# Optimization experiments

Measured on AMD Instinct MI355X. Metric: run time of the kernel, lower is better.

Reference implementation:

```python
import jax, jax.numpy as jnp
from jax import lax
import numpy as np

D_MODEL, D_STATE, D_CONV, EXPAND = 1024, 16, 4, 2
D_INNER = EXPAND * D_MODEL          # 2048
DT_RANK = D_MODEL // 16             # 64
B_SZ, L_SEQ = 2, 2048


def setup_inputs() -> dict:
    key = jax.random.key(0)
    ks = jax.random.split(key, 8)
    x = jax.random.normal(ks[0], (B_SZ, L_SEQ, D_MODEL), jnp.float32)
    inp = {
        "x": x,
        "ln_g": jnp.ones((D_MODEL,), jnp.float32),
        "ln_b": jnp.zeros((D_MODEL,), jnp.float32),
        # fan-in scaled weights for numerical sanity
        "W_in": jax.random.normal(ks[1], (2 * D_INNER, D_MODEL), jnp.float32) / np.sqrt(D_MODEL),
        "conv_w": jax.random.normal(ks[2], (D_INNER, D_CONV), jnp.float32) / np.sqrt(D_CONV),
        "conv_b": jnp.zeros((D_INNER,), jnp.float32),
        "W_xp": jax.random.normal(ks[3], (DT_RANK + 2 * D_STATE, D_INNER), jnp.float32) / np.sqrt(D_INNER),
        "W_dt": jax.random.normal(ks[4], (D_INNER, DT_RANK), jnp.float32) / np.sqrt(DT_RANK),
        "b_dt": jax.random.normal(ks[5], (D_INNER,), jnp.float32) * 0.1 - 4.0,  # softplus(dt) small, like mamba init
        # S4D-real init: A = -exp(A_log), A_log = log(1..d_state)
        "A_log": jnp.broadcast_to(jnp.log(jnp.arange(1, D_STATE + 1, dtype=jnp.float32)), (D_INNER, D_STATE)).copy(),
        "D": jnp.ones((D_INNER,), jnp.float32),
        "W_out": jax.random.normal(ks[6], (D_MODEL, D_INNER), jnp.float32) / np.sqrt(D_INNER),
    }
    return inp


def _selective_scan(u, dt, A, Bm, Cm, Dvec):
    # u, dt: (B, L, d_inner); Bm, Cm: (B, L, d_state); A: (d_inner, d_state)
    def step(h, inputs):
        u_t, dt_t, B_t, C_t = inputs                      # (B,di),(B,di),(B,n),(B,n)
        dA = jnp.exp(dt_t[:, :, None] * A[None])          # (B,di,n), in (0,1) since A<0
        dBu = (dt_t * u_t)[:, :, None] * B_t[:, None, :]  # (B,di,n)
        h = dA * h + dBu
        y = jnp.einsum('bdn,bn->bd', h, C_t)
        return h, y
    xs = (u.transpose(1, 0, 2), dt.transpose(1, 0, 2),
          Bm.transpose(1, 0, 2), Cm.transpose(1, 0, 2))
    h0 = jnp.zeros((u.shape[0], u.shape[2], A.shape[1]), u.dtype)
    _, ys = lax.scan(step, h0, xs)
    return ys.transpose(1, 0, 2) + u * Dvec               # (B, L, d_inner)


def reference(x, ln_g, ln_b, W_in, conv_w, conv_b, W_xp, W_dt, b_dt, A_log, D, W_out):
    d_inner, d_conv = conv_w.shape
    dt_rank = W_dt.shape[1]
    d_state = A_log.shape[1]
    # pre-LayerNorm
    mu = jnp.mean(x, axis=-1, keepdims=True)
    var = jnp.mean(jnp.square(x - mu), axis=-1, keepdims=True)
    xn = (x - mu) * lax.rsqrt(var + 1e-5) * ln_g + ln_b
    # input projection -> (B, L, 2*d_inner)
    xz = jnp.einsum('bld,ed->ble', xn, W_in)
    u, z = jnp.split(xz, 2, axis=-1)
    # causal depthwise conv over time
    u_c = lax.conv_general_dilated(
        u.transpose(0, 2, 1),                 # (B, d_inner, L)
        conv_w[:, None, :],                   # (d_inner, 1, d_conv)
        window_strides=(1,), padding=[(d_conv - 1, 0)],
        feature_group_count=d_inner)
    u_c = jax.nn.silu((u_c + conv_b[None, :, None]).transpose(0, 2, 1))  # (B, L, d_inner)
    # data-dependent dt, B, C
    x_dbl = jnp.einsum('bld,ed->ble', u_c, W_xp)
    dt, Bm, Cm = jnp.split(x_dbl, [dt_rank, dt_rank + d_state], axis=-1)
    dt = jax.nn.softplus(jnp.einsum('blr,dr->bld', dt, W_dt) + b_dt)
    A = -jnp.exp(A_log)
    y = _selective_scan(u_c, dt, A, Bm, Cm, D)
    y = y * jax.nn.silu(z)
    out = jnp.einsum('ble,de->bld', y, W_out)
    return x + out
```

## Files before the change

### kernel.cpp

```cpp
#include <hip/hip_runtime.h>

typedef __bf16 bf16x8 __attribute__((ext_vector_type(8)));
typedef float  f32x4  __attribute__((ext_vector_type(4)));

#define LOG2E 1.44269504088896f

__device__ __forceinline__ float bfl(unsigned short s) {
    return __uint_as_float(((unsigned int)s) << 16);
}
__device__ __forceinline__ unsigned short f2bf(float f) {
    unsigned int x = __float_as_uint(f);
    x += 0x7fffu + ((x >> 16) & 1u);
    return (unsigned short)(x >> 16);
}
__device__ __forceinline__ float fexp2(float x) { return __builtin_amdgcn_exp2f(x); }
__device__ __forceinline__ float fexp(float x)  { return __builtin_amdgcn_exp2f(x * LOG2E); }
__device__ __forceinline__ float frcp(float x)  { return __builtin_amdgcn_rcpf(x); }
__device__ __forceinline__ float silu_f(float x) {
    return x * frcp(1.f + fexp2(-x * LOG2E));
}
__device__ __forceinline__ void gl_lds(const unsigned short* g, unsigned short* l) {
    __builtin_amdgcn_global_load_lds(
        (__attribute__((address_space(1))) const void*)g,
        (__attribute__((address_space(3))) void*)l, 16, 0, 0);
}

#define BSZ   2
#define LSEQ  2048
#define DMODEL 1024
#define DI    2048
#define DS    16
#define NCH   64
#define CL    32

#define WI_N   4194304
#define WXP_N  196608
#define WDT_N  131072
#define WOUT_N 2097152
#define WSEG1  (WI_N)
#define WSEG2  (WI_N + WXP_N)
#define WSEG3  (WI_N + WXP_N + WDT_N)
#define WTOT   (WI_N + WXP_N + WDT_N + WOUT_N)

__global__ __launch_bounds__(256) void cvt_weights(
    const float* __restrict__ w0, const float* __restrict__ w1,
    const float* __restrict__ w2, const float* __restrict__ w3,
    unsigned short* __restrict__ dst)
{
    const size_t e0 = ((size_t)blockIdx.x * 256 + threadIdx.x) * 8;
    if (e0 >= WTOT) return;
    const float* src;
    size_t off;
    if      (e0 < WSEG1) { src = w0; off = e0; }
    else if (e0 < WSEG2) { src = w1; off = e0 - WSEG1; }
    else if (e0 < WSEG3) { src = w2; off = e0 - WSEG2; }
    else                 { src = w3; off = e0 - WSEG3; }
    float4 a = *(const float4*)(src + off);
    float4 b = *(const float4*)(src + off + 4);
    ushort4 lo, hi;
    lo.x = f2bf(a.x); lo.y = f2bf(a.y); lo.z = f2bf(a.z); lo.w = f2bf(a.w);
    hi.x = f2bf(b.x); hi.y = f2bf(b.y); hi.z = f2bf(b.z); hi.w = f2bf(b.w);
    *(ushort4*)(dst + e0) = lo;
    *(ushort4*)(dst + e0 + 4) = hi;
}

__global__ __launch_bounds__(256) void ln_kernel(
    const float* __restrict__ x,
    const float* __restrict__ g,
    const float* __restrict__ b,
    unsigned short* __restrict__ xn)
{
    const int row = blockIdx.x;
    const int tid = threadIdx.x;
    const int lane = tid & 63, wv = tid >> 6;
    const float* xp = x + (size_t)row * DMODEL;

    float4 v = ((const float4*)xp)[tid];
    float s = v.x + v.y + v.z + v.w;
    float q = v.x*v.x + v.y*v.y + v.z*v.z + v.w*v.w;
    #pragma unroll
    for (int o = 32; o > 0; o >>= 1) {
        s += __shfl_down(s, o);
        q += __shfl_down(q, o);
    }
    __shared__ float ss[4], sq[4];
    if (lane == 0) { ss[wv] = s; sq[wv] = q; }
    __syncthreads();
    s = ss[0] + ss[1] + ss[2] + ss[3];
    q = sq[0] + sq[1] + sq[2] + sq[3];
    const float mu  = s * (1.f / DMODEL);
    const float var = q * (1.f / DMODEL) - mu * mu;
    const float rs  = rsqrtf(var + 1e-5f);

    float4 gv = ((const float4*)g)[tid];
    float4 bv = ((const float4*)b)[tid];
    ushort4 o;
    o.x = f2bf((v.x - mu) * rs * gv.x + bv.x);
    o.y = f2bf((v.y - mu) * rs * gv.y + bv.y);
    o.z = f2bf((v.z - mu) * rs * gv.z + bv.z);
    o.w = f2bf((v.w - mu) * rs * gv.w + bv.w);
    ((ushort4*)(xn + (size_t)row * DMODEL))[tid] = o;
}

template<int EPI, int LOGM>
__global__ __launch_bounds__(512, 2) void gemm_pipe256(
    const unsigned short* __restrict__ A,
    const unsigned short* __restrict__ Bw,
    void* __restrict__ Cout,
    const void* __restrict__ aux0,
    int K, int ldc)
{
    __shared__ unsigned short As[2][256 * 64];
    __shared__ unsigned short Bs[2][256 * 64];
    const int tid  = threadIdx.x;
    const int lane = tid & 63;
    const int wid  = tid >> 6;
    const int wm   = (wid >> 2) * 128;
    const int wn   = (wid & 3) * 64;

    const int nwg = gridDim.x;
    const int id  = blockIdx.x;
    const int swz = (id & 7) * (nwg >> 3) + (id >> 3);
    const int bx  = swz & ((1 << LOGM) - 1);
    const int by  = swz >> LOGM;
    const size_t am0 = (size_t)bx * 256;
    const size_t bn0 = (size_t)by * 256;

    const int srow  = lane >> 3;
    const int sslot = (lane & 7) ^ srow;
    const unsigned short* gA = A  + (am0 + wid * 8 + srow) * (size_t)K + sslot * 8;
    const unsigned short* gB = Bw + (bn0 + wid * 8 + srow) * (size_t)K + sslot * 8;

    const int NT = K >> 6;

#define STAGE256(buf, ko)                                                      \
    {   _Pragma("unroll")                                                      \
        for (int j = 0; j < 4; ++j)                                            \
            gl_lds(gA + (size_t)(j * 64) * K + (ko), &As[buf][(j * 64 + wid * 8) * 64]); \
        _Pragma("unroll")                                                      \
        for (int j = 0; j < 4; ++j)                                            \
            gl_lds(gB + (size_t)(j * 64) * K + (ko), &Bs[buf][(j * 64 + wid * 8) * 64]); }

    STAGE256(0, 0)
    STAGE256(1, 64)

    f32x4 acc[8][4];
    f32x4 z4 = {0.f, 0.f, 0.f, 0.f};
    #pragma unroll
    for (int i = 0; i < 8; ++i)
        #pragma unroll
        for (int j = 0; j < 4; ++j) acc[i][j] = z4;

    const int lr  = lane & 15;
    const int lq  = lane >> 4;
    const int key = lr & 7;

#define RD_A(dst, q)                                                           \
    _Pragma("unroll")                                                          \
    for (int i = 0; i < 2; ++i)                                                \
        _Pragma("unroll")                                                      \
        for (int ks = 0; ks < 2; ++ks)                                         \
            dst[i][ks] = *(const bf16x8*)&As[cur][(wm + ((q) * 2 + i) * 16 + lr) * 64 \
                                                  + (((ks * 4 + lq) ^ key) * 8)];

#define MFMA_Q(src, q)                                                         \
    _Pragma("unroll")                                                          \
    for (int i = 0; i < 2; ++i)                                                \
        _Pragma("unroll")                                                      \
        for (int fn = 0; fn < 4; ++fn) {                                       \
            acc[(q) * 2 + i][fn] = __builtin_amdgcn_mfma_f32_16x16x32_bf16(    \
                src[i][0], bfv[fn][0], acc[(q) * 2 + i][fn], 0, 0, 0);         \
            acc[(q) * 2 + i][fn] = __builtin_amdgcn_mfma_f32_16x16x32_bf16(    \
                src[i][1], bfv[fn][1], acc[(q) * 2 + i][fn], 0, 0, 0);         }

    for (int t = 0; t < NT; ++t) {
        const int cur = t & 1;
        if (t < NT - 1) asm volatile("s_waitcnt vmcnt(8)" ::: "memory");
        else            asm volatile("s_waitcnt vmcnt(0)" ::: "memory");
        __builtin_amdgcn_s_barrier();
        __builtin_amdgcn_sched_barrier(0);

        bf16x8 bfv[4][2], fA[2][2], fB[2][2];
        #pragma unroll
        for (int fn = 0; fn < 4; ++fn)
            #pragma unroll
            for (int ks = 0; ks < 2; ++ks)
                bfv[fn][ks] = *(const bf16x8*)&Bs[cur][(wn + fn * 16 + lr) * 64
                                                        + (((ks * 4 + lq) ^ key) * 8)];
        RD_A(fA, 0)
        asm volatile("s_waitcnt lgkmcnt(0)" ::: "memory");
        __builtin_amdgcn_sched_barrier(0);

        RD_A(fB, 1)
        __builtin_amdgcn_s_setprio(1);
        MFMA_Q(fA, 0)
        __builtin_amdgcn_s_setprio(0);
        asm volatile("s_waitcnt lgkmcnt(0)" ::: "memory");
        __builtin_amdgcn_sched_barrier(0);

        RD_A(fA, 2)
        __builtin_amdgcn_s_setprio(1);
        MFMA_Q(fB, 1)
        __builtin_amdgcn_s_setprio(0);
        asm volatile("s_waitcnt lgkmcnt(0)" ::: "memory");
        __builtin_amdgcn_sched_barrier(0);

        RD_A(fB, 3)
        __builtin_amdgcn_s_setprio(1);
        MFMA_Q(fA, 2)
        __builtin_amdgcn_s_setprio(0);
        asm volatile("s_waitcnt lgkmcnt(0)" ::: "memory");
        __builtin_amdgcn_sched_barrier(0);

        __builtin_amdgcn_s_barrier();
        if (t + 2 < NT) {
            STAGE256(cur, (size_t)(t + 2) * 64)
        }
        __builtin_amdgcn_s_setprio(1);
        MFMA_Q(fB, 3)
        __builtin_amdgcn_s_setprio(0);
    }
#undef RD_A
#undef MFMA_Q
#undef STAGE256

    const int er = lq * 4;
    const int ec = lr;
    #pragma unroll
    for (int fm = 0; fm < 8; ++fm) {
        #pragma unroll
        for (int fn = 0; fn < 4; ++fn) {
            const size_t col = bn0 + wn + fn * 16 + ec;
            #pragma unroll
            for (int r = 0; r < 4; ++r) {
                const size_t row = am0 + wm + fm * 16 + er + r;
                float v = acc[fm][fn][r];
                if constexpr (EPI == 0) {
                    ((unsigned short*)Cout)[row * ldc + col] = f2bf(v);
                } else {
                    float t2 = v + ((const float*)aux0)[row * ldc + col];
                    ((float*)Cout)[row * ldc + col] = t2;
                }
            }
        }
    }
}

template<int BM, int BN, int EPI, int LOG_NBXM>
__global__ __launch_bounds__(256) void gemm_lds(
    const unsigned short* __restrict__ A,
    const unsigned short* __restrict__ Bw,
    void* __restrict__ Cout,
    const void* __restrict__ aux0,
    int K, int ldc)
{
    constexpr int FM = BM / 32;
    constexpr int FN = BN / 32;
    __shared__ unsigned short As[BM * 64];
    __shared__ unsigned short Bs[BN * 64];
    const int tid  = threadIdx.x;
    const int lane = tid & 63;
    const int wv   = tid >> 6;
    const int wm   = (wv >> 1) * (BM / 2);
    const int wn   = (wv & 1)  * (BN / 2);

    const int nwg = gridDim.x;
    const int id  = blockIdx.x;
    const int swz = (id & 7) * (nwg >> 3) + (id >> 3);
    const int bx  = swz & ((1 << LOG_NBXM) - 1);
    const int by  = swz >> LOG_NBXM;

    f32x4 acc[FM][FN];
    f32x4 z4 = {0.f, 0.f, 0.f, 0.f};
    #pragma unroll
    for (int i = 0; i < FM; ++i)
        #pragma unroll
        for (int j = 0; j < FN; ++j) acc[i][j] = z4;

    const size_t am0 = (size_t)bx * BM;
    const size_t bn0 = (size_t)by * BN;
    const int srow  = lane >> 3;
    const int scol  = (lane & 7) * 8;

    for (int k0 = 0; k0 < K; k0 += 64) {
        __syncthreads();
        #pragma unroll
        for (int i = 0; i < BM / 32; ++i) {
            const int rb = (wv * (BM / 32) + i) * 8;
            gl_lds(&A[(am0 + rb + srow) * (size_t)K + k0 + scol], &As[rb * 64]);
        }
        #pragma unroll
        for (int i = 0; i < BN / 32; ++i) {
            const int rb = (wv * (BN / 32) + i) * 8;
            gl_lds(&Bw[(bn0 + rb + srow) * (size_t)K + k0 + scol], &Bs[rb * 64]);
        }
        __syncthreads();
        const int lr = lane & 15, lk = (lane >> 4) * 8;
        #pragma unroll
        for (int ks = 0; ks < 2; ++ks) {
            bf16x8 af[FM], bfv[FN];
            #pragma unroll
            for (int fm = 0; fm < FM; ++fm)
                af[fm] = *(const bf16x8*)&As[(wm + fm * 16 + lr) * 64 + ks * 32 + lk];
            #pragma unroll
            for (int fn = 0; fn < FN; ++fn)
                bfv[fn] = *(const bf16x8*)&Bs[(wn + fn * 16 + lr) * 64 + ks * 32 + lk];
            #pragma unroll
            for (int fm = 0; fm < FM; ++fm)
                #pragma unroll
                for (int fn = 0; fn < FN; ++fn)
                    acc[fm][fn] = __builtin_amdgcn_mfma_f32_16x16x32_bf16(
                        af[fm], bfv[fn], acc[fm][fn], 0, 0, 0);
        }
    }

    const int er = (lane >> 4) * 4;
    const int ec = lane & 15;
    #pragma unroll
    for (int fm = 0; fm < FM; ++fm) {
        #pragma unroll
        for (int fn = 0; fn < FN; ++fn) {
            const size_t col = bn0 + wn + fn * 16 + ec;
            #pragma unroll
            for (int r = 0; r < 4; ++r) {
                const size_t row = am0 + wm + fm * 16 + er + r;
                float v = acc[fm][fn][r];
                if constexpr (EPI == 0) {
                    ((unsigned short*)Cout)[row * ldc + col] = f2bf(v);
                } else if constexpr (EPI == 2) {
                    float t = v + ((const float*)aux0)[col];
                    float e = fexp2(t * LOG2E);
                    float sp = 0.69314718056f * __builtin_amdgcn_logf(1.f + e);
                    if (t > 20.f) sp = t;
                    ((unsigned short*)Cout)[row * ldc + col] = f2bf(sp);
                } else {
                    float t = v + ((const float*)aux0)[row * ldc + col];
                    ((float*)Cout)[row * ldc + col] = t;
                }
            }
        }
    }
}

__global__ __launch_bounds__(256) void gemm4_splitk(
    const unsigned short* __restrict__ A,
    const unsigned short* __restrict__ Bw,
    float* __restrict__ Cpart)
{
    constexpr int LDP = 72;
    __shared__ unsigned short As[64 * LDP];
    __shared__ unsigned short Bs[96 * LDP];
    const int tid  = threadIdx.x;
    const int lane = tid & 63;
    const int wv   = tid >> 6;
    const int wm   = (wv >> 1) * 32;
    const int wn   = (wv & 1)  * 48;

    f32x4 acc[2][3];
    f32x4 z4 = {0.f, 0.f, 0.f, 0.f};
    #pragma unroll
    for (int i = 0; i < 2; ++i)
        #pragma unroll
        for (int j = 0; j < 3; ++j) acc[i][j] = z4;

    const size_t am0 = (size_t)blockIdx.x * 64;
    const int kz = blockIdx.y;
    const int kbeg = kz * 256;
    const int r0 = tid >> 3;
    const int c0 = (tid & 7) * 8;

    for (int k0 = kbeg; k0 < kbeg + 256; k0 += 64) {
        __syncthreads();
        #pragma unroll
        for (int p = 0; p < 2; ++p) {
            int r = r0 + p * 32;
            *(uint4*)&As[r * LDP + c0] = *(const uint4*)&A[(am0 + r) * (size_t)2048 + k0 + c0];
        }
        #pragma unroll
        for (int p = 0; p < 3; ++p) {
            int r = r0 + p * 32;
            *(uint4*)&Bs[r * LDP + c0] = *(const uint4*)&Bw[(size_t)r * 2048 + k0 + c0];
        }
        __syncthreads();
        const int lr = lane & 15, lk = (lane >> 4) * 8;
        #pragma unroll
        for (int ks = 0; ks < 2; ++ks) {
            bf16x8 af[2], bfv[3];
            #pragma unroll
            for (int fm = 0; fm < 2; ++fm)
                af[fm] = *(const bf16x8*)&As[(wm + fm * 16 + lr) * LDP + ks * 32 + lk];
            #pragma unroll
            for (int fn = 0; fn < 3; ++fn)
                bfv[fn] = *(const bf16x8*)&Bs[(wn + fn * 16 + lr) * LDP + ks * 32 + lk];
            #pragma unroll
            for (int fm = 0; fm < 2; ++fm)
                #pragma unroll
                for (int fn = 0; fn < 3; ++fn)
                    acc[fm][fn] = __builtin_amdgcn_mfma_f32_16x16x32_bf16(
                        af[fm], bfv[fn], acc[fm][fn], 0, 0, 0);
        }
    }

    const int er = (lane >> 4) * 4;
    const int ec = lane & 15;
    float* out = Cpart + (size_t)kz * 4096 * 96;
    #pragma unroll
    for (int fm = 0; fm < 2; ++fm) {
        #pragma unroll
        for (int fn = 0; fn < 3; ++fn) {
            const int col = wn + fn * 16 + ec;
            #pragma unroll
            for (int r = 0; r < 4; ++r) {
                const size_t row = am0 + wm + fm * 16 + er + r;
                out[row * 96 + col] = acc[fm][fn][r];
            }
        }
    }
}

__global__ __launch_bounds__(256) void reduce_xdbl(
    const float* __restrict__ Cpart,
    float* __restrict__ x_dbl,
    unsigned short* __restrict__ dtlow)
{
    const int e = blockIdx.x * 256 + threadIdx.x;
    float s = 0.f;
    #pragma unroll
    for (int kz = 0; kz < 8; ++kz) s += Cpart[(size_t)kz * 393216 + e];
    x_dbl[e] = s;
    const int row = e / 96, col = e - row * 96;
    if (col < 64) dtlow[row * 64 + col] = f2bf(s);
}

__global__ __launch_bounds__(256) void conv_silu(
    const unsigned short* __restrict__ xz,
    const float* __restrict__ convw,
    const float* __restrict__ convb,
    unsigned short* __restrict__ u_c)
{
    const size_t i = (size_t)blockIdx.x * 256 + threadIdx.x;
    if (i >= (size_t)BSZ * LSEQ * DI) return;
    const int d = (int)(i & (DI - 1));
    const size_t bl = i >> 11;
    const int l = (int)(bl & (LSEQ - 1));
    const int b = (int)(bl >> 11);

    float4 wv = *(const float4*)&convw[d * 4];
    float acc = convb[d];
    const size_t rowbase = (size_t)(b * LSEQ) * (2 * DI) + d;
    if (l >= 3) acc += bfl(xz[rowbase + (size_t)(l - 3) * (2 * DI)]) * wv.x;
    if (l >= 2) acc += bfl(xz[rowbase + (size_t)(l - 2) * (2 * DI)]) * wv.y;
    if (l >= 1) acc += bfl(xz[rowbase + (size_t)(l - 1) * (2 * DI)]) * wv.z;
    acc += bfl(xz[rowbase + (size_t)l * (2 * DI)]) * wv.w;
    u_c[i] = f2bf(silu_f(acc));
}

__device__ __forceinline__ bool load_A(const float* __restrict__ A_log, int d, float* An2) {
    bool fast = true;
    #pragma unroll
    for (int i = 0; i < 4; ++i) {
        float4 a = *(const float4*)&A_log[(size_t)d * DS + i * 4];
        float e0 = fexp(a.x), e1 = fexp(a.y), e2 = fexp(a.z), e3 = fexp(a.w);
        fast = fast && fabsf(e0 - (4*i+1)) < 1e-3f * (4*i+1)
                    && fabsf(e1 - (4*i+2)) < 1e-3f * (4*i+2)
                    && fabsf(e2 - (4*i+3)) < 1e-3f * (4*i+3)
                    && fabsf(e3 - (4*i+4)) < 1e-3f * (4*i+4);
        An2[4*i+0] = -e0 * LOG2E; An2[4*i+1] = -e1 * LOG2E;
        An2[4*i+2] = -e2 * LOG2E; An2[4*i+3] = -e3 * LOG2E;
    }
    return fast;
}

__global__ __launch_bounds__(256) void scan1(
    const unsigned short* __restrict__ dt,
    const unsigned short* __restrict__ u_c,
    const float* __restrict__ x_dbl,
    const float* __restrict__ A_log,
    float* __restrict__ chunk_h,
    float* __restrict__ Ssum)
{
    const int d = blockIdx.x * 256 + threadIdx.x;
    const int b = blockIdx.y, c = blockIdx.z;
    const int tid = threadIdx.x;

    __shared__ float sB[CL][DS];
    if (tid < 128) {
        int s = tid >> 2, j = (tid & 3) * 4;
        *(float4*)&sB[s][j] =
            *(const float4*)&x_dbl[(size_t)(b * LSEQ + c * CL + s) * 96 + 64 + j];
    }

    float An2[DS];
    const bool fast = load_A(A_log, d, An2);
    __syncthreads();

    float h[DS];
    #pragma unroll
    for (int n = 0; n < DS; ++n) h[n] = 0.f;
    float S = 0.f;
    const size_t base = (size_t)(b * LSEQ + c * CL) * DI + d;
    if (fast) {
        for (int s = 0; s < CL; ++s) {
            float dtt = bfl(dt[base + (size_t)s * DI]);
            float ut  = bfl(u_c[base + (size_t)s * DI]);
            S += dtt;
            float dtu = dtt * ut;
            float e1 = fexp2(-dtt * LOG2E);
            float p = 1.f;
            #pragma unroll
            for (int n = 0; n < DS; ++n) {
                p *= e1;
                h[n] = p * h[n] + dtu * sB[s][n];
            }
        }
    } else {
        for (int s = 0; s < CL; ++s) {
            float dtt = bfl(dt[base + (size_t)s * DI]);
            float ut  = bfl(u_c[base + (size_t)s * DI]);
            S += dtt;
            float dtu = dtt * ut;
            #pragma unroll
            for (int n = 0; n < DS; ++n) {
                float dA = fexp2(dtt * An2[n]);
                h[n] = dA * h[n] + dtu * sB[s][n];
            }
        }
    }
    const size_t co = ((size_t)((b * NCH + c) * DI) + d) * DS;
    #pragma unroll
    for (int n = 0; n < DS; ++n) chunk_h[co + n] = h[n];
    Ssum[(size_t)(b * NCH + c) * DI + d] = S;
}

__global__ __launch_bounds__(256) void scan2(
    float* __restrict__ chunk_h,
    const float* __restrict__ Ssum,
    const float* __restrict__ A_log)
{
    const int gid = blockIdx.x * 256 + threadIdx.x;
    const int b = gid >> 15;
    const int rem = gid & 32767;
    const int d = rem >> 4;
    const int n = rem & 15;
    const float A2 = -fexp(A_log[(size_t)d * DS + n]) * LOG2E;
    float H = 0.f;
    for (int c = 0; c < NCH; ++c) {
        const size_t idx = ((size_t)((b * NCH + c) * DI) + d) * DS + n;
        float hl = chunk_h[idx];
        float S  = Ssum[(size_t)(b * NCH + c) * DI + d];
        chunk_h[idx] = H;
        H = fexp2(A2 * S) * H + hl;
    }
}

__global__ __launch_bounds__(256) void scan3(
    const unsigned short* __restrict__ dt,
    const unsigned short* __restrict__ u_c,
    const float* __restrict__ x_dbl,
    const float* __restrict__ A_log,
    const float* __restrict__ Hstart,
    const float* __restrict__ Dvec,
    const unsigned short* __restrict__ xz,
    unsigned short* __restrict__ yb)
{
    const int d = blockIdx.x * 256 + threadIdx.x;
    const int b = blockIdx.y, c = blockIdx.z;
    const int tid = threadIdx.x;

    __shared__ float sBC[CL][32];
    {
        int s = tid >> 3, j = (tid & 7) * 4;
        *(float4*)&sBC[s][j] =
            *(const float4*)&x_dbl[(size_t)(b * LSEQ + c * CL + s) * 96 + 64 + j];
    }

    float An2[DS];
    const bool fast = load_A(A_log, d, An2);
    const float Dd = Dvec[d];
    float h[DS];
    const size_t co = ((size_t)((b * NCH + c) * DI) + d) * DS;
    #pragma unroll
    for (int n = 0; n < DS; ++n) h[n] = Hstart[co + n];
    __syncthreads();

    const size_t base  = (size_t)(b * LSEQ + c * CL) * DI + d;
    const size_t zbase = (size_t)(b * LSEQ + c * CL) * (2 * DI) + DI + d;
    if (fast) {
        for (int s = 0; s < CL; ++s) {
            float dtt = bfl(dt[base + (size_t)s * DI]);
            float ut  = bfl(u_c[base + (size_t)s * DI]);
            float dtu = dtt * ut;
            float e1 = fexp2(-dtt * LOG2E);
            float p = 1.f;
            float a0 = 0.f, a1 = 0.f;
            #pragma unroll
            for (int n = 0; n < DS; ++n) {
                p *= e1;
                h[n] = p * h[n] + dtu * sBC[s][n];
                if (n & 1) a1 += h[n] * sBC[s][16 + n];
                else       a0 += h[n] * sBC[s][16 + n];
            }
            float y = a0 + a1 + Dd * ut;
            float z = bfl(xz[zbase + (size_t)s * (2 * DI)]);
            yb[base + (size_t)s * DI] = f2bf(y * silu_f(z));
        }
    } else {
        for (int s = 0; s < CL; ++s) {
            float dtt = bfl(dt[base + (size_t)s * DI]);
            float ut  = bfl(u_c[base + (size_t)s * DI]);
            float dtu = dtt * ut;
            float a0 = 0.f, a1 = 0.f;
            #pragma unroll
            for (int n = 0; n < DS; ++n) {
                float dA = fexp2(dtt * An2[n]);
                h[n] = dA * h[n] + dtu * sBC[s][n];
                if (n & 1) a1 += h[n] * sBC[s][16 + n];
                else       a0 += h[n] * sBC[s][16 + n];
            }
            float y = a0 + a1 + Dd * ut;
            float z = bfl(xz[zbase + (size_t)s * (2 * DI)]);
            yb[base + (size_t)s * DI] = f2bf(y * silu_f(z));
        }
    }
}

extern "C" void kernel_launch(void* const* d_in, const int* in_sizes, int n_in,
                              void* d_out, int out_size, void* d_ws, size_t ws_size,
                              hipStream_t stream) {
    const float* x      = (const float*)d_in[0];
    const float* ln_g   = (const float*)d_in[1];
    const float* ln_b   = (const float*)d_in[2];
    const float* W_in   = (const float*)d_in[3];
    const float* conv_w = (const float*)d_in[4];
    const float* conv_b = (const float*)d_in[5];
    const float* W_xp   = (const float*)d_in[6];
    const float* W_dt   = (const float*)d_in[7];
    const float* b_dt   = (const float*)d_in[8];
    const float* A_log  = (const float*)d_in[9];
    const float* Dv     = (const float*)d_in[10];
    const float* W_out  = (const float*)d_in[11];
    float* out = (float*)d_out;

    char* w = (char*)d_ws;
    unsigned short* xn     = (unsigned short*)(w + 0);
    unsigned short* xz     = (unsigned short*)(w + 8388608);
    unsigned short* u_c    = (unsigned short*)(w + 41943040);
    float*          x_dbl  = (float*)         (w + 58720256);
    unsigned short* dtlow  = (unsigned short*)(w + 60293120);
    unsigned short* dtb    = (unsigned short*)(w + 60817408);
    float*          chunkh = (float*)         (w + 77594624);
    float*          Ssum   = (float*)         (w + 94371840);
    unsigned short* yb     = (unsigned short*)(w + 95420416);
    unsigned short* wbf    = (unsigned short*)(w + 112197632);
    float*          Cpart  = (float*)         (w + 125435904);
    unsigned short* Wi_bf   = wbf;
    unsigned short* Wxp_bf  = wbf + WSEG1;
    unsigned short* Wdt_bf  = wbf + WSEG2;
    unsigned short* Wout_bf = wbf + WSEG3;
    (void)in_sizes; (void)n_in; (void)out_size; (void)ws_size;

    const int MROWS = BSZ * LSEQ;

    cvt_weights<<<(WTOT / 8 + 255) / 256, 256, 0, stream>>>(
        W_in, W_xp, W_dt, W_out, wbf);
    ln_kernel<<<MROWS, 256, 0, stream>>>(x, ln_g, ln_b, xn);
    gemm_pipe256<0, 4><<<256, 512, 0, stream>>>(
        xn, Wi_bf, xz, nullptr, DMODEL, 2 * DI);
    conv_silu<<<(MROWS * DI) / 256, 256, 0, stream>>>(xz, conv_w, conv_b, u_c);
    gemm4_splitk<<<dim3(64, 8), 256, 0, stream>>>(u_c, Wxp_bf, Cpart);
    reduce_xdbl<<<(MROWS * 96) / 256, 256, 0, stream>>>(Cpart, x_dbl, dtlow);
    gemm_lds<128, 64, 2, 5><<<1024, 256, 0, stream>>>(
        dtlow, Wdt_bf, dtb, b_dt, 64, DI);
    scan1<<<dim3(DI / 256, BSZ, NCH), 256, 0, stream>>>(
        dtb, u_c, x_dbl, A_log, chunkh, Ssum);
    scan2<<<(BSZ * DI * DS) / 256, 256, 0, stream>>>(chunkh, Ssum, A_log);
    scan3<<<dim3(DI / 256, BSZ, NCH), 256, 0, stream>>>(
        dtb, u_c, x_dbl, A_log, chunkh, Dv, xz, yb);
    gemm_lds<128, 64, 3, 5><<<512, 256, 0, stream>>>(
        yb, Wout_bf, out, x, DI, DMODEL);
}
```

Measured before the change: 195.3 us.

## Use pipelined 128x128 MFMA GEMM kernel for output projection

Adds a new gemm_pipe128 kernel with 8 waves per 128x128 tile. It double-buffers direct global-to-LDS loads with XOR-swizzled layout and interleaves LDS reads with MFMA using sched barriers and priority hints. It replaces the gemm_lds 128x64 kernel used for the output projection with residual add. This aims to hide memory latency and raise MFMA utilization, at the cost of fewer workgroups (256) and more LDS per block.

```diff
diff --git a/kernel.cpp b/kernel.cpp
--- a/kernel.cpp
+++ b/kernel.cpp
@@ -230,6 +230,134 @@
     for (int fm = 0; fm < 8; ++fm) {
         #pragma unroll
         for (int fn = 0; fn < 4; ++fn) {
+            const size_t col = bn0 + wn + fn * 16 + ec;
+            #pragma unroll
+            for (int r = 0; r < 4; ++r) {
+                const size_t row = am0 + wm + fm * 16 + er + r;
+                float v = acc[fm][fn][r];
+                if constexpr (EPI == 0) {
+                    ((unsigned short*)Cout)[row * ldc + col] = f2bf(v);
+                } else {
+                    float t2 = v + ((const float*)aux0)[row * ldc + col];
+                    ((float*)Cout)[row * ldc + col] = t2;
+                }
+            }
+        }
+    }
+}
+
+template<int EPI, int LOGNB>
+__global__ __launch_bounds__(512, 2) void gemm_pipe128(
+    const unsigned short* __restrict__ A,
+    const unsigned short* __restrict__ Bw,
+    void* __restrict__ Cout,
+    const void* __restrict__ aux0,
+    int K, int ldc)
+{
+    __shared__ unsigned short As[2][128 * 64];
+    __shared__ unsigned short Bs[2][128 * 64];
+    const int tid  = threadIdx.x;
+    const int lane = tid & 63;
+    const int wid  = tid >> 6;
+    const int wm   = (wid >> 2) * 64;
+    const int wn   = (wid & 3) * 32;
+
+    const int nwg = gridDim.x;
+    const int id  = blockIdx.x;
+    const int swz = (id & 7) * (nwg >> 3) + (id >> 3);
+    const int bn_i = swz & ((1 << LOGNB) - 1);
+    const int bm_i = swz >> LOGNB;
+    const size_t am0 = (size_t)bm_i * 128;
+    const size_t bn0 = (size_t)bn_i * 128;
+
+    const int srow  = lane >> 3;
+    const int sslot = (lane & 7) ^ srow;
+    const unsigned short* gA = A  + (am0 + wid * 16 + srow) * (size_t)K + sslot * 8;
+    const unsigned short* gB = Bw + (bn0 + wid * 16 + srow) * (size_t)K + sslot * 8;
+
+    const int NT = K >> 6;
+
+#define STAGE128(buf, ko)                                                      \
+    {   _Pragma("unroll")                                                      \
+        for (int j = 0; j < 2; ++j)                                            \
+            gl_lds(gA + (size_t)(j * 8) * K + (ko), &As[buf][(wid * 16 + j * 8) * 64]); \
+        _Pragma("unroll")                                                      \
+        for (int j = 0; j < 2; ++j)                                            \
+            gl_lds(gB + (size_t)(j * 8) * K + (ko), &Bs[buf][(wid * 16 + j * 8) * 64]); }
+
+    STAGE128(0, 0)
+    STAGE128(1, 64)
+
+    f32x4 acc[4][2];
+    f32x4 z4 = {0.f, 0.f, 0.f, 0.f};
+    #pragma unroll
+    for (int i = 0; i < 4; ++i) { acc[i][0] = z4; acc[i][1] = z4; }
+
+    const int lr  = lane & 15;
+    const int lq  = lane >> 4;
+    const int key = lr & 7;
+
+#define RD_A128(dst, h)                                                        \
+    _Pragma("unroll")                                                          \
+    for (int i = 0; i < 2; ++i)                                                \
+        _Pragma("unroll")                                                      \
+        for (int ks = 0; ks < 2; ++ks)                                         \
+            dst[i][ks] = *(const bf16x8*)&As[cur][(wm + ((h) * 2 + i) * 16 + lr) * 64 \
+                                                  + (((ks * 4 + lq) ^ key) * 8)];
+
+#define MFMA_H(src, h)                                                         \
+    _Pragma("unroll")                                                          \
+    for (int i = 0; i < 2; ++i)                                                \
+        _Pragma("unroll")                                                      \
+        for (int fn = 0; fn < 2; ++fn) {                                       \
+            acc[(h) * 2 + i][fn] = __builtin_amdgcn_mfma_f32_16x16x32_bf16(    \
+                src[i][0], bfv[fn][0], acc[(h) * 2 + i][fn], 0, 0, 0);         \
+            acc[(h) * 2 + i][fn] = __builtin_amdgcn_mfma_f32_16x16x32_bf16(    \
+                src[i][1], bfv[fn][1], acc[(h) * 2 + i][fn], 0, 0, 0);         }
+
+    for (int t = 0; t < NT; ++t) {
+        const int cur = t & 1;
+        if (t < NT - 1) asm volatile("s_waitcnt vmcnt(4)" ::: "memory");
+        else            asm volatile("s_waitcnt vmcnt(0)" ::: "memory");
+        __builtin_amdgcn_s_barrier();
+        __builtin_amdgcn_sched_barrier(0);
+
+        bf16x8 bfv[2][2], fA[2][2], fB[2][2];
+        #pragma unroll
+        for (int fn = 0; fn < 2; ++fn)
+            #pragma unroll
+            for (int ks = 0; ks < 2; ++ks)
+                bfv[fn][ks] = *(const bf16x8*)&Bs[cur][(wn + fn * 16 + lr) * 64
+                                                        + (((ks * 4 + lq) ^ key) * 8)];
+        RD_A128(fA, 0)
+        asm volatile("s_waitcnt lgkmcnt(0)" ::: "memory");
+        __builtin_amdgcn_sched_barrier(0);
+
+        RD_A128(fB, 1)
+        __builtin_amdgcn_s_setprio(1);
+        MFMA_H(fA, 0)
+        __builtin_amdgcn_s_setprio(0);
+        asm volatile("s_waitcnt lgkmcnt(0)" ::: "memory");
+        __builtin_amdgcn_sched_barrier(0);
+
+        __builtin_amdgcn_s_barrier();
+        if (t + 2 < NT) {
+            STAGE128(cur, (size_t)(t + 2) * 64)
+        }
+        __builtin_amdgcn_s_setprio(1);
+        MFMA_H(fB, 1)
+        __builtin_amdgcn_s_setprio(0);
+    }
+#undef RD_A128
+#undef MFMA_H
+#undef STAGE128
+
+    const int er = lq * 4;
+    const int ec = lr;
+    #pragma unroll
+    for (int fm = 0; fm < 4; ++fm) {
+        #pragma unroll
+        for (int fn = 0; fn < 2; ++fn) {
             const size_t col = bn0 + wn + fn * 16 + ec;
             #pragma unroll
             for (int r = 0; r < 4; ++r) {
@@ -676,6 +804,6 @@
     scan2<<<(BSZ * DI * DS) / 256, 256, 0, stream>>>(chunkh, Ssum, A_log);
     scan3<<<dim3(DI / 256, BSZ, NCH), 256, 0, stream>>>(
         dtb, u_c, x_dbl, A_log, chunkh, Dv, xz, yb);
-    gemm_lds<128, 64, 3, 5><<<512, 256, 0, stream>>>(
+    gemm_pipe128<3, 3><<<256, 512, 0, stream>>>(
         yb, Wout_bf, out, x, DI, DMODEL);
 }
```

Result: faster. 182.4 us (-6.6%).
